# Kernel tuning notes

Hardware: AMD Instinct MI355X
Metric: run time of the kernel (lower is better)

Reference implementation:

```python
import jax, jax.numpy as jnp
import numpy as np

B, N, E, K = 8, 4096, 1, 3
F = [16, 32, 16]
MLP_HID, MLP_OUT = 64, 1


def graph_filter(x, S, h, b):
    # x: [B, Fin, N], S: [E, N, N], h: [Fout, E, K, Fin], b: [Fout, 1]
    Bx, Fin, Nx = x.shape
    Ex, Kx = h.shape[1], h.shape[2]
    cur = jnp.broadcast_to(x[:, None], (Bx, Ex, Fin, Nx))  # tap 0: z = x
    zs = [cur]
    for _ in range(Kx - 1):
        cur = jnp.einsum('enm,befm->befn', S, cur)  # diffuse one hop
        zs.append(cur)
    z = jnp.stack(zs, axis=2)  # [B, E, K, Fin, N]
    return jnp.einsum('gekf,bekfn->bgn', h, z) + b[None]  # [B, Fout, N]


def gnn_layer(x, S, h, b, n_out):
    # GraphFilter -> ReLU -> NoPool (select first n_out nodes)
    return jax.nn.relu(graph_filter(x, S, h, b))[:, :, :n_out]


def setup_inputs() -> dict:
    key = jax.random.key(0)
    ks = jax.random.split(key, 16)
    sN = np.float32(1.0 / np.sqrt(N))
    x = jax.random.normal(ks[0], (B, F[0], N), dtype=jnp.float32)
    S_clique = jax.random.normal(ks[1], (E, N, N), dtype=jnp.float32) * sN
    S_line = jax.random.normal(ks[2], (E, N, N), dtype=jnp.float32) * sN

    def w(k, fo, fi):
        s = np.float32(1.0 / np.sqrt(fi * K))
        return jax.random.normal(k, (fo, E, K, fi), dtype=jnp.float32) * s

    Wc1, bc1 = w(ks[3], F[1], F[0]), jnp.zeros((F[1], 1), jnp.float32)
    Wc2, bc2 = w(ks[4], F[2], F[1]), jnp.zeros((F[2], 1), jnp.float32)
    Wl1, bl1 = w(ks[5], F[1], F[0]), jnp.zeros((F[1], 1), jnp.float32)
    Wl2, bl2 = w(ks[6], F[2], F[1]), jnp.zeros((F[2], 1), jnp.float32)
    d_in = N * F[-1]
    Wm1 = jax.random.normal(ks[7], (MLP_HID, d_in), dtype=jnp.float32) * np.float32(1.0 / np.sqrt(d_in))
    bm1 = jnp.zeros((MLP_HID,), jnp.float32)
    Wm2 = jax.random.normal(ks[8], (MLP_OUT, MLP_HID), dtype=jnp.float32) * np.float32(1.0 / np.sqrt(MLP_HID))
    bm2 = jnp.zeros((MLP_OUT,), jnp.float32)
    return {'x': x, 'S_clique': S_clique, 'S_line': S_line,
            'Wc1': Wc1, 'bc1': bc1, 'Wc2': Wc2, 'bc2': bc2,
            'Wl1': Wl1, 'bl1': bl1, 'Wl2': Wl2, 'bl2': bl2,
            'Wm1': Wm1, 'bm1': bm1, 'Wm2': Wm2, 'bm2': bm2}


def reference(x, S_clique, S_line, Wc1, bc1, Wc2, bc2, Wl1, bl1, Wl2, bl2, Wm1, bm1, Wm2, bm2):
    # clique-expansion branch (L=2 layers)
    y = gnn_layer(x, S_clique, Wc1, bc1, N)
    y = gnn_layer(y, S_clique, Wc2, bc2, N)
    # line-expansion branch (L=2 layers)
    y = gnn_layer(y, S_line, Wl1, bl1, N)
    y = gnn_layer(y, S_line, Wl2, bl2, N)
    yFlat = y.reshape(y.shape[0], -1)  # [B, F[-1]*N] (row-major matches torch)
    h = jax.nn.relu(yFlat @ Wm1.T + bm1)
    return h @ Wm2.T + bm2  # [B, 1]
```

## Files before the change

kernel.cpp:

```cpp
#include <hip/hip_runtime.h>


#define NN 4096
#define BB 8

typedef unsigned short u16;
typedef unsigned int   u32;

typedef __attribute__((ext_vector_type(8))) short bf16x8;
typedef __attribute__((ext_vector_type(4))) float f32x4;

__device__ __forceinline__ u16 f2bf(float f) {
    union { float f; u32 i; } c; c.f = f;
    u32 i = c.i;
    u32 r = (i + 0x7FFFu + ((i >> 16) & 1u)) >> 16;
    return (u16)r;
}
__device__ __forceinline__ float bf2f(u16 u) {
    union { u32 i; float f; } c; c.i = ((u32)u) << 16; return c.f;
}

__device__ __forceinline__ void gload_lds16(const u16* g, u16* l) {
    __builtin_amdgcn_global_load_lds(
        (__attribute__((address_space(1))) void*)g,
        (__attribute__((address_space(3))) void*)l, 16, 0, 0);
}

__global__ __launch_bounds__(256) void cvt_f32_bf16(const float* __restrict__ in,
                                                    u16* __restrict__ out, int n)
{
    int i = (blockIdx.x * 256 + threadIdx.x) * 4;
    const int stride = gridDim.x * 256 * 4;
    for (; i < n; i += stride) {
        float4 v = *(const float4*)(in + i);
        ushort4 o;
        o.x = f2bf(v.x); o.y = f2bf(v.y); o.z = f2bf(v.z); o.w = f2bf(v.w);
        *(ushort4*)(out + i) = o;
    }
}

__global__ __launch_bounds__(256) void diffuse(const u16* __restrict__ Z,
                                               const u16* __restrict__ S,
                                               u16* __restrict__ Part)
{
    __shared__ u16 As[128 * 64];
    __shared__ u16 Bs[64 * 64];

    const int bx    = blockIdx.x;
    const int ntile = ((bx & 7) << 3) | (bx >> 3);
    const int nBase = ntile * 64;
    const int mBase = blockIdx.y * 128;
    const int tid   = threadIdx.x;
    const int lane  = tid & 63;
    const int wv    = tid >> 6;
    const int quad  = lane >> 4;
    const int l16   = lane & 15;

    const int kSlice = NN / (int)gridDim.z;
    const int kStart = (int)blockIdx.z * kSlice;

    const int rl   = lane >> 3;
    const int gsl  = lane & 7;
    const int gsrc = gsl ^ rl;

    f32x4 acc[2][4];
#pragma unroll
    for (int i = 0; i < 2; ++i)
#pragma unroll
        for (int j = 0; j < 4; ++j) acc[i][j] = (f32x4){0.f, 0.f, 0.f, 0.f};

    for (int k0 = kStart; k0 < kStart + kSlice; k0 += 64) {
#pragma unroll
        for (int j = 0; j < 4; ++j) {
            const int rb = (wv * 4 + j) * 8;
            gload_lds16(Z + (size_t)(mBase + rb + rl) * NN + k0 + gsrc * 8,
                        &As[rb * 64]);
        }
#pragma unroll
        for (int j = 0; j < 2; ++j) {
            const int rb = (wv * 2 + j) * 8;
            gload_lds16(S + (size_t)(nBase + rb + rl) * NN + k0 + gsrc * 8,
                        &Bs[rb * 64]);
        }
        __syncthreads();

#pragma unroll
        for (int s = 0; s < 2; ++s) {
            const int g = s * 4 + quad;
            bf16x8 af[2], bf[4];
#pragma unroll
            for (int mi = 0; mi < 2; ++mi) {
                const int r = wv * 32 + mi * 16 + l16;
                af[mi] = *(const bf16x8*)&As[r * 64 + ((g ^ (r & 7)) << 3)];
            }
#pragma unroll
            for (int ni = 0; ni < 4; ++ni) {
                const int r = ni * 16 + l16;
                bf[ni] = *(const bf16x8*)&Bs[r * 64 + ((g ^ (r & 7)) << 3)];
            }
#pragma unroll
            for (int mi = 0; mi < 2; ++mi)
#pragma unroll
                for (int ni = 0; ni < 4; ++ni)
                    acc[mi][ni] = __builtin_amdgcn_mfma_f32_16x16x32_bf16(
                        af[mi], bf[ni], acc[mi][ni], 0, 0, 0);
        }
        __syncthreads();
    }

    const size_t plane = (size_t)gridDim.y * 128 * NN;
    u16* pp = Part + (size_t)blockIdx.z * plane;
#pragma unroll
    for (int mi = 0; mi < 2; ++mi)
#pragma unroll
        for (int ni = 0; ni < 4; ++ni) {
            const int row0 = mBase + wv * 32 + mi * 16 + quad * 4;
            const int col  = nBase + ni * 16 + l16;
#pragma unroll
            for (int i = 0; i < 4; ++i)
                pp[(size_t)(row0 + i) * NN + col] = f2bf(acc[mi][ni][i]);
        }
}

template <int KS>
__global__ __launch_bounds__(256) void reduce_part(const u16* __restrict__ part,
                                                   int planeElems,
                                                   u16* __restrict__ outb)
{
    const int base   = (blockIdx.x * 256 + threadIdx.x) * 8;
    const int stride = gridDim.x * 256 * 8;
    for (int i = base; i < planeElems; i += stride) {
        float s[8];
#pragma unroll
        for (int e = 0; e < 8; ++e) s[e] = 0.f;
#pragma unroll
        for (int p = 0; p < KS; ++p) {
            uint4 v = *(const uint4*)(part + (size_t)p * planeElems + i);
            const u32 w[4] = {v.x, v.y, v.z, v.w};
#pragma unroll
            for (int q = 0; q < 4; ++q) {
                union { u32 i; float f; } lo, hi;
                lo.i = w[q] << 16;
                hi.i = w[q] & 0xFFFF0000u;
                s[q * 2]     += lo.f;
                s[q * 2 + 1] += hi.f;
            }
        }
        uint4 o;
        o.x = (u32)f2bf(s[0]) | ((u32)f2bf(s[1]) << 16);
        o.y = (u32)f2bf(s[2]) | ((u32)f2bf(s[3]) << 16);
        o.z = (u32)f2bf(s[4]) | ((u32)f2bf(s[5]) << 16);
        o.w = (u32)f2bf(s[6]) | ((u32)f2bf(s[7]) << 16);
        *(uint4*)(outb + i) = o;
    }
}

template <int FIN, int FOUT>
__global__ __launch_bounds__(256) void combine_relu(
    const u16* __restrict__ z0, const u16* __restrict__ z1,
    const u16* __restrict__ z2, const float* __restrict__ W,
    const float* __restrict__ bias, u16* __restrict__ out)
{
    __shared__ float hs[FOUT * 3 * FIN];
    __shared__ float bs[FOUT];
    for (int i = threadIdx.x; i < FOUT * 3 * FIN; i += 256) hs[i] = W[i];
    if (threadIdx.x < FOUT) bs[threadIdx.x] = bias[threadIdx.x];
    __syncthreads();

    const int nb = NN / 256;
    const int b  = blockIdx.x / nb;
    const int n  = (blockIdx.x % nb) * 256 + threadIdx.x;

    float zv[3][FIN];
    const u16* zp0 = z0 + (size_t)b * FIN * NN + n;
    const u16* zp1 = z1 + (size_t)b * FIN * NN + n;
    const u16* zp2 = z2 + (size_t)b * FIN * NN + n;
#pragma unroll
    for (int f = 0; f < FIN; ++f) {
        zv[0][f] = bf2f(zp0[(size_t)f * NN]);
        zv[1][f] = bf2f(zp1[(size_t)f * NN]);
        zv[2][f] = bf2f(zp2[(size_t)f * NN]);
    }

    u16* op = out + (size_t)b * FOUT * NN + n;
    for (int g = 0; g < FOUT; ++g) {
        float acc = bs[g];
#pragma unroll
        for (int k = 0; k < 3; ++k)
#pragma unroll
            for (int f = 0; f < FIN; ++f)
                acc = fmaf(hs[(g * 3 + k) * FIN + f], zv[k][f], acc);
        op[(size_t)g * NN] = f2bf(fmaxf(acc, 0.f));
    }
}

__global__ __launch_bounds__(256) void mlp1(const u16* __restrict__ y,
                                            const float* __restrict__ Wm1,
                                            float* __restrict__ h1raw)
{
    const int j    = blockIdx.x;
    const int base = blockIdx.y * 8192;
    const int D    = 16 * NN;

    float acc[BB];
#pragma unroll
    for (int b = 0; b < BB; ++b) acc[b] = 0.f;

    const float* wrow = Wm1 + (size_t)j * D + base;
    for (int idx = threadIdx.x * 8; idx < 8192; idx += 256 * 8) {
        float4 w0 = *(const float4*)(wrow + idx);
        float4 w1 = *(const float4*)(wrow + idx + 4);
#pragma unroll
        for (int b = 0; b < BB; ++b) {
            uint4 yv = *(const uint4*)(y + (size_t)b * D + base + idx);
            union { u32 i; float f; } c[8];
            c[0].i = yv.x << 16; c[1].i = yv.x & 0xFFFF0000u;
            c[2].i = yv.y << 16; c[3].i = yv.y & 0xFFFF0000u;
            c[4].i = yv.z << 16; c[5].i = yv.z & 0xFFFF0000u;
            c[6].i = yv.w << 16; c[7].i = yv.w & 0xFFFF0000u;
            acc[b] = fmaf(w0.x, c[0].f, acc[b]);
            acc[b] = fmaf(w0.y, c[1].f, acc[b]);
            acc[b] = fmaf(w0.z, c[2].f, acc[b]);
            acc[b] = fmaf(w0.w, c[3].f, acc[b]);
            acc[b] = fmaf(w1.x, c[4].f, acc[b]);
            acc[b] = fmaf(w1.y, c[5].f, acc[b]);
            acc[b] = fmaf(w1.z, c[6].f, acc[b]);
            acc[b] = fmaf(w1.w, c[7].f, acc[b]);
        }
    }

    __shared__ float red[BB][4];
    const int lane = threadIdx.x & 63;
    const int w    = threadIdx.x >> 6;
#pragma unroll
    for (int b = 0; b < BB; ++b) {
        float v = acc[b];
        for (int off = 32; off > 0; off >>= 1) v += __shfl_down(v, off, 64);
        if (lane == 0) red[b][w] = v;
    }
    __syncthreads();
    if (threadIdx.x < BB) {
        const int b = threadIdx.x;
        atomicAdd(&h1raw[b * 64 + j],
                  red[b][0] + red[b][1] + red[b][2] + red[b][3]);
    }
}

__global__ void mlp2(const float* __restrict__ h1raw,
                     const float* __restrict__ bm1,
                     const float* __restrict__ Wm2,
                     const float* __restrict__ bm2, float* __restrict__ out)
{
    const int lane = threadIdx.x;
    const float w    = Wm2[lane];
    const float b1   = bm1[lane];
    const float bias = bm2[0];
    for (int b = 0; b < BB; ++b) {
        float v = fmaxf(h1raw[b * 64 + lane] + b1, 0.f) * w;
        for (int off = 32; off > 0; off >>= 1) v += __shfl_down(v, off, 64);
        if (lane == 0) out[b] = v + bias;
    }
}

extern "C" void kernel_launch(void* const* d_in, const int* in_sizes, int n_in,
                              void* d_out, int out_size, void* d_ws, size_t ws_size,
                              hipStream_t stream)
{
    const float* x   = (const float*)d_in[0];
    const float* Sc  = (const float*)d_in[1];
    const float* Sl  = (const float*)d_in[2];
    const float* Wc1 = (const float*)d_in[3];
    const float* bc1 = (const float*)d_in[4];
    const float* Wc2 = (const float*)d_in[5];
    const float* bc2 = (const float*)d_in[6];
    const float* Wl1 = (const float*)d_in[7];
    const float* bl1 = (const float*)d_in[8];
    const float* Wl2 = (const float*)d_in[9];
    const float* bl2 = (const float*)d_in[10];
    const float* Wm1 = (const float*)d_in[11];
    const float* bm1 = (const float*)d_in[12];
    const float* Wm2 = (const float*)d_in[13];
    const float* bm2 = (const float*)d_in[14];
    float* out = (float*)d_out;

    char* ws = (char*)d_ws;
    u16*   part = (u16*)(ws);
    u16*   zb1  = (u16*)(ws + (8u  << 20));
    u16*   zb2  = (u16*)(ws + (10u << 20));
    u16*   yPa  = (u16*)(ws + (12u << 20));
    u16*   yPb  = (u16*)(ws + (14u << 20));
    float* h1   = (float*)(ws + (16u << 20));
    u16*   Scb  = (u16*)(ws + (17u << 20));
    u16*   Slb  = Scb + (size_t)NN * NN;

    const dim3 blk(256);
    const dim3 gridCmb(BB * NN / 256);
    const dim3 g2(64, 1, 8);
    const dim3 g4(64, 2, 4);
    const int  pl128 = 128 * NN;
    const int  pl256 = 256 * NN;

    cvt_f32_bf16<<<1024, blk, 0, stream>>>(Sc, Scb, NN * NN);
    cvt_f32_bf16<<<1024, blk, 0, stream>>>(Sl, Slb, NN * NN);
    cvt_f32_bf16<<<512, blk, 0, stream>>>(x, yPa, 128 * NN);

    diffuse<<<g2, blk, 0, stream>>>(yPa, Scb, part);
    reduce_part<8><<<256, blk, 0, stream>>>(part, pl128, zb1);
    diffuse<<<g2, blk, 0, stream>>>(zb1, Scb, part);
    reduce_part<8><<<256, blk, 0, stream>>>(part, pl128, zb2);
    combine_relu<16, 32><<<gridCmb, blk, 0, stream>>>(yPa, zb1, zb2, Wc1, bc1, yPb);
    diffuse<<<g4, blk, 0, stream>>>(yPb, Scb, part);
    reduce_part<4><<<512, blk, 0, stream>>>(part, pl256, zb1);
    diffuse<<<g4, blk, 0, stream>>>(zb1, Scb, part);
    reduce_part<4><<<512, blk, 0, stream>>>(part, pl256, zb2);
    combine_relu<32, 16><<<gridCmb, blk, 0, stream>>>(yPb, zb1, zb2, Wc2, bc2, yPa);
    diffuse<<<g2, blk, 0, stream>>>(yPa, Slb, part);
    reduce_part<8><<<256, blk, 0, stream>>>(part, pl128, zb1);
    diffuse<<<g2, blk, 0, stream>>>(zb1, Slb, part);
    reduce_part<8><<<256, blk, 0, stream>>>(part, pl128, zb2);
    combine_relu<16, 32><<<gridCmb, blk, 0, stream>>>(yPa, zb1, zb2, Wl1, bl1, yPb);
    diffuse<<<g4, blk, 0, stream>>>(yPb, Slb, part);
    reduce_part<4><<<512, blk, 0, stream>>>(part, pl256, zb1);
    diffuse<<<g4, blk, 0, stream>>>(zb1, Slb, part);
    reduce_part<4><<<512, blk, 0, stream>>>(part, pl256, zb2);
    combine_relu<32, 16><<<gridCmb, blk, 0, stream>>>(yPb, zb1, zb2, Wl2, bl2, yPa);
    hipMemsetAsync(h1, 0, 64 * BB * sizeof(float), stream);
    mlp1<<<dim3(64, 8), blk, 0, stream>>>(yPa, Wm1, h1);
    mlp2<<<1, 64, 0, stream>>>(h1, bm1, Wm2, bm2, out);
}
```

Measured before the change: 399.8 us.

## Double-buffer diffuse LDS tiles and fuse second split-K reduce into combine

Result: faster. 388.0 us (-3.0%).

```diff
diff --git a/kernel.cpp b/kernel.cpp
--- a/kernel.cpp
+++ b/kernel.cpp
@@ -43,8 +43,8 @@
                                                const u16* __restrict__ S,
                                                u16* __restrict__ Part)
 {
-    __shared__ u16 As[128 * 64];
-    __shared__ u16 Bs[64 * 64];
+    __shared__ u16 As[2][128 * 64];
+    __shared__ u16 Bs[2][64 * 64];
 
     const int bx    = blockIdx.x;
     const int ntile = ((bx & 7) << 3) | (bx >> 3);
@@ -58,6 +58,7 @@
 
     const int kSlice = NN / (int)gridDim.z;
     const int kStart = (int)blockIdx.z * kSlice;
+    const int iters  = kSlice / 64;
 
     const int rl   = lane >> 3;
     const int gsl  = lane & 7;
@@ -69,21 +70,22 @@
 #pragma unroll
         for (int j = 0; j < 4; ++j) acc[i][j] = (f32x4){0.f, 0.f, 0.f, 0.f};
 
-    for (int k0 = kStart; k0 < kStart + kSlice; k0 += 64) {
+    auto stage = [&](int buf, int k0) {
 #pragma unroll
         for (int j = 0; j < 4; ++j) {
             const int rb = (wv * 4 + j) * 8;
             gload_lds16(Z + (size_t)(mBase + rb + rl) * NN + k0 + gsrc * 8,
-                        &As[rb * 64]);
+                        &As[buf][rb * 64]);
         }
 #pragma unroll
         for (int j = 0; j < 2; ++j) {
             const int rb = (wv * 2 + j) * 8;
             gload_lds16(S + (size_t)(nBase + rb + rl) * NN + k0 + gsrc * 8,
-                        &Bs[rb * 64]);
-        }
-        __syncthreads();
-
+                        &Bs[buf][rb * 64]);
+        }
+    };
+
+    auto compute = [&](int buf) {
 #pragma unroll
         for (int s = 0; s < 2; ++s) {
             const int g = s * 4 + quad;
@@ -91,12 +93,12 @@
 #pragma unroll
             for (int mi = 0; mi < 2; ++mi) {
                 const int r = wv * 32 + mi * 16 + l16;
-                af[mi] = *(const bf16x8*)&As[r * 64 + ((g ^ (r & 7)) << 3)];
+                af[mi] = *(const bf16x8*)&As[buf][r * 64 + ((g ^ (r & 7)) << 3)];
             }
 #pragma unroll
             for (int ni = 0; ni < 4; ++ni) {
                 const int r = ni * 16 + l16;
-                bf[ni] = *(const bf16x8*)&Bs[r * 64 + ((g ^ (r & 7)) << 3)];
+                bf[ni] = *(const bf16x8*)&Bs[buf][r * 64 + ((g ^ (r & 7)) << 3)];
             }
 #pragma unroll
             for (int mi = 0; mi < 2; ++mi)
@@ -105,8 +107,19 @@
                     acc[mi][ni] = __builtin_amdgcn_mfma_f32_16x16x32_bf16(
                         af[mi], bf[ni], acc[mi][ni], 0, 0, 0);
         }
+    };
+
+    stage(0, kStart);
+    __syncthreads();
+
+    int cur = 0;
+    for (int i = 0; i < iters - 1; ++i) {
+        stage(cur ^ 1, kStart + (i + 1) * 64);
+        compute(cur);
         __syncthreads();
-    }
+        cur ^= 1;
+    }
+    compute(cur);
 
     const size_t plane = (size_t)gridDim.y * 128 * NN;
     u16* pp = Part + (size_t)blockIdx.z * plane;
@@ -155,11 +168,12 @@
     }
 }
 
-template <int FIN, int FOUT>
+template <int FIN, int FOUT, int KS>
 __global__ __launch_bounds__(256) void combine_relu(
     const u16* __restrict__ z0, const u16* __restrict__ z1,
-    const u16* __restrict__ z2, const float* __restrict__ W,
-    const float* __restrict__ bias, u16* __restrict__ out)
+    const u16* __restrict__ part2, int planeElems,
+    const float* __restrict__ W, const float* __restrict__ bias,
+    u16* __restrict__ out)
 {
     __shared__ float hs[FOUT * 3 * FIN];
     __shared__ float bs[FOUT];
@@ -174,12 +188,16 @@
     float zv[3][FIN];
     const u16* zp0 = z0 + (size_t)b * FIN * NN + n;
     const u16* zp1 = z1 + (size_t)b * FIN * NN + n;
-    const u16* zp2 = z2 + (size_t)b * FIN * NN + n;
+    const u16* zp2 = part2 + (size_t)b * FIN * NN + n;
 #pragma unroll
     for (int f = 0; f < FIN; ++f) {
         zv[0][f] = bf2f(zp0[(size_t)f * NN]);
         zv[1][f] = bf2f(zp1[(size_t)f * NN]);
-        zv[2][f] = bf2f(zp2[(size_t)f * NN]);
+        float s = 0.f;
+#pragma unroll
+        for (int p = 0; p < KS; ++p)
+            s += bf2f(zp2[(size_t)p * planeElems + (size_t)f * NN]);
+        zv[2][f] = s;
     }
 
     u16* op = out + (size_t)b * FOUT * NN + n;
@@ -196,7 +214,7 @@
 
 __global__ __launch_bounds__(256) void mlp1(const u16* __restrict__ y,
                                             const float* __restrict__ Wm1,
-                                            float* __restrict__ h1raw)
+                                            float* __restrict__ h1p)
 {
     const int j    = blockIdx.x;
     const int base = blockIdx.y * 8192;
@@ -241,12 +259,12 @@
     __syncthreads();
     if (threadIdx.x < BB) {
         const int b = threadIdx.x;
-        atomicAdd(&h1raw[b * 64 + j],
-                  red[b][0] + red[b][1] + red[b][2] + red[b][3]);
-    }
-}
-
-__global__ void mlp2(const float* __restrict__ h1raw,
+        h1p[blockIdx.y * (BB * 64) + b * 64 + j] =
+            red[b][0] + red[b][1] + red[b][2] + red[b][3];
+    }
+}
+
+__global__ void mlp2(const float* __restrict__ h1p,
                      const float* __restrict__ bm1,
                      const float* __restrict__ Wm2,
                      const float* __restrict__ bm2, float* __restrict__ out)
@@ -256,7 +274,10 @@
     const float b1   = bm1[lane];
     const float bias = bm2[0];
     for (int b = 0; b < BB; ++b) {
-        float v = fmaxf(h1raw[b * 64 + lane] + b1, 0.f) * w;
+        float h = 0.f;
+#pragma unroll
+        for (int p = 0; p < 8; ++p) h += h1p[p * (BB * 64) + b * 64 + lane];
+        float v = fmaxf(h + b1, 0.f) * w;
         for (int off = 32; off > 0; off >>= 1) v += __shfl_down(v, off, 64);
         if (lane == 0) out[b] = v + bias;
     }
@@ -286,10 +307,9 @@
     char* ws = (char*)d_ws;
     u16*   part = (u16*)(ws);
     u16*   zb1  = (u16*)(ws + (8u  << 20));
-    u16*   zb2  = (u16*)(ws + (10u << 20));
     u16*   yPa  = (u16*)(ws + (12u << 20));
     u16*   yPb  = (u16*)(ws + (14u << 20));
-    float* h1   = (float*)(ws + (16u << 20));
+    float* h1p  = (float*)(ws + (16u << 20));
     u16*   Scb  = (u16*)(ws + (17u << 20));
     u16*   Slb  = Scb + (size_t)NN * NN;
 
@@ -307,24 +327,23 @@
     diffuse<<<g2, blk, 0, stream>>>(yPa, Scb, part);
     reduce_part<8><<<256, blk, 0, stream>>>(part, pl128, zb1);
     diffuse<<<g2, blk, 0, stream>>>(zb1, Scb, part);
-    reduce_part<8><<<256, blk, 0, stream>>>(part, pl128, zb2);
-    combine_relu<16, 32><<<gridCmb, blk, 0, stream>>>(yPa, zb1, zb2, Wc1, bc1, yPb);
+    combine_relu<16, 32, 8><<<gridCmb, blk, 0, stream>>>(yPa, zb1, part, pl128,
+                                                         Wc1, bc1, yPb);
     diffuse<<<g4, blk, 0, stream>>>(yPb, Scb, part);
     reduce_part<4><<<512, blk, 0, stream>>>(part, pl256, zb1);
     diffuse<<<g4, blk, 0, stream>>>(zb1, Scb, part);
-    reduce_part<4><<<512, blk, 0, stream>>>(part, pl256, zb2);
-    combine_relu<32, 16><<<gridCmb, blk, 0, stream>>>(yPb, zb1, zb2, Wc2, bc2, yPa);
+    combine_relu<32, 16, 4><<<gridCmb, blk, 0, stream>>>(yPb, zb1, part, pl256,
+                                                         Wc2, bc2, yPa);
     diffuse<<<g2, blk, 0, stream>>>(yPa, Slb, part);
     reduce_part<8><<<256, blk, 0, stream>>>(part, pl128, zb1);
     diffuse<<<g2, blk, 0, stream>>>(zb1, Slb, part);
-    reduce_part<8><<<256, blk, 0, stream>>>(part, pl128, zb2);
-    combine_relu<16, 32><<<gridCmb, blk, 0, stream>>>(yPa, zb1, zb2, Wl1, bl1, yPb);
+    combine_relu<16, 32, 8><<<gridCmb, blk, 0, stream>>>(yPa, zb1, part, pl128,
+                                                         Wl1, bl1, yPb);
     diffuse<<<g4, blk, 0, stream>>>(yPb, Slb, part);
     reduce_part<4><<<512, blk, 0, stream>>>(part, pl256, zb1);
     diffuse<<<g4, blk, 0, stream>>>(zb1, Slb, part);
-    reduce_part<4><<<512, blk, 0, stream>>>(part, pl256, zb2);
-    combine_relu<32, 16><<<gridCmb, blk, 0, stream>>>(yPb, zb1, zb2, Wl2, bl2, yPa);
-    hipMemsetAsync(h1, 0, 64 * BB * sizeof(float), stream);
-    mlp1<<<dim3(64, 8), blk, 0, stream>>>(yPa, Wm1, h1);
-    mlp2<<<1, 64, 0, stream>>>(h1, bm1, Wm2, bm2, out);
-}
+    combine_relu<32, 16, 4><<<gridCmb, blk, 0, stream>>>(yPb, zb1, part, pl256,
+                                                         Wl2, bl2, yPa);
+    mlp1<<<dim3(64, 8), blk, 0, stream>>>(yPa, Wm1, h1p);
+    mlp2<<<1, 64, 0, stream>>>(h1p, bm1, Wm2, bm2, out);
+}
```
